# Optimization experiments

Hardware: AMD Instinct MI355X
Metric: run time of the kernel (lower is better)

The kernel has to match this reference:

```python
import jax, jax.numpy as jnp
import numpy as np

B, N = 1, 768
C_A, C_S, C_Z = 768, 384, 128
H, C_HID, N_TRANS = 16, 48, 2
INF = 1e9
PNAMES = ['attn_s_ln_g', 'attn_ada_gate_w', 'attn_ada_gate_b', 'attn_ada_skip_w',
          'wq', 'bq', 'wk', 'wv', 'z_ln_g', 'z_ln_b', 'wb', 'wg', 'wo',
          'attn_out_gate_w', 'attn_out_gate_b',
          'tr_s_ln_g', 'tr_ada_gate_w', 'tr_ada_gate_b', 'tr_ada_skip_w',
          'tr_w1', 'tr_w2', 'tr_wo', 'tr_out_gate_w', 'tr_out_gate_b']


def _ln(x, eps=1e-5):
    mu = jnp.mean(x, axis=-1, keepdims=True)
    var = jnp.mean((x - mu) ** 2, axis=-1, keepdims=True)
    return (x - mu) * jax.lax.rsqrt(var + eps)


def _adaln(a, s, s_g, gate_w, gate_b, skip_w):
    # AF3 Algorithm 26 AdaLN: a <- LN(a, no affine); s <- LN(s, scale only)
    a_ln = _ln(a)
    s_ln = _ln(s) * s_g
    return jax.nn.sigmoid(s_ln @ gate_w + gate_b) * a_ln + s_ln @ skip_w


def setup_inputs() -> dict:
    key = jax.random.key(0)
    ks = iter(jax.random.split(key, 40))
    w = lambda *sh: jax.random.normal(next(ks), sh, jnp.float32) * 0.02
    return dict(
        a=jax.random.normal(next(ks), (B, N, C_A), jnp.float32),
        s=jax.random.normal(next(ks), (B, N, C_S), jnp.float32),
        z=jax.random.normal(next(ks), (B, N, N, C_Z), jnp.float32),
        mask=jnp.ones((B, N), jnp.int32),
        attn_s_ln_g=jnp.ones((C_S,), jnp.float32),
        attn_ada_gate_w=w(C_S, C_A),
        attn_ada_gate_b=jnp.zeros((C_A,), jnp.float32),
        attn_ada_skip_w=w(C_S, C_A),
        wq=w(C_A, H * C_HID), bq=jnp.zeros((H * C_HID,), jnp.float32),
        wk=w(C_A, H * C_HID), wv=w(C_A, H * C_HID),
        z_ln_g=jnp.ones((C_Z,), jnp.float32), z_ln_b=jnp.zeros((C_Z,), jnp.float32),
        wb=w(C_Z, H), wg=w(C_A, H * C_HID), wo=w(H * C_HID, C_A),
        attn_out_gate_w=w(C_S, C_A),
        attn_out_gate_b=jnp.full((C_A,), -2.0, jnp.float32),  # AdaLN-Zero bias init -2
        tr_s_ln_g=jnp.ones((C_S,), jnp.float32),
        tr_ada_gate_w=w(C_S, C_A),
        tr_ada_gate_b=jnp.zeros((C_A,), jnp.float32),
        tr_ada_skip_w=w(C_S, C_A),
        tr_w1=w(C_A, N_TRANS * C_A), tr_w2=w(C_A, N_TRANS * C_A),
        tr_wo=w(N_TRANS * C_A, C_A),
        tr_out_gate_w=w(C_S, C_A),
        tr_out_gate_b=jnp.full((C_A,), -2.0, jnp.float32),
    )


def _block(a, s, z, maskf, p):
    # --- AttentionPairBias (AF3 Alg 24), residual ---
    a_ln = _adaln(a, s, p['attn_s_ln_g'], p['attn_ada_gate_w'],
                  p['attn_ada_gate_b'], p['attn_ada_skip_w'])
    q = (a_ln @ p['wq'] + p['bq']).reshape(B, N, H, C_HID)
    k = (a_ln @ p['wk']).reshape(B, N, H, C_HID)
    v = (a_ln @ p['wv']).reshape(B, N, H, C_HID)
    pair_bias = (_ln(z) * p['z_ln_g'] + p['z_ln_b']) @ p['wb']  # [B,N,N,H]
    logits = jnp.einsum('bqhc,bkhc->bhqk', q, k) / np.float32(np.sqrt(C_HID))
    logits = logits + jnp.moveaxis(pair_bias, -1, 1)
    logits = logits + (maskf - 1.0)[:, None, None, :] * INF  # mask over keys
    attn = jax.nn.softmax(logits, axis=-1)
    o = jnp.einsum('bhqk,bkhc->bqhc', attn, v)
    g = jax.nn.sigmoid(a_ln @ p['wg']).reshape(B, N, H, C_HID)
    o = (o * g).reshape(B, N, H * C_HID) @ p['wo']
    o = jax.nn.sigmoid(s @ p['attn_out_gate_w'] + p['attn_out_gate_b']) * o
    a = a + o
    # --- ConditionedTransitionBlock (AF3 Alg 25, SwiGLU), residual ---
    t_ln = _adaln(a, s, p['tr_s_ln_g'], p['tr_ada_gate_w'],
                  p['tr_ada_gate_b'], p['tr_ada_skip_w'])
    hid = jax.nn.silu(t_ln @ p['tr_w1']) * (t_ln @ p['tr_w2'])
    t = jax.nn.sigmoid(s @ p['tr_out_gate_w'] + p['tr_out_gate_b']) * (hid @ p['tr_wo'])
    t = t * maskf[..., None]  # _mask_trans=True
    return a + t


def reference(a, s, z, mask, attn_s_ln_g, attn_ada_gate_w, attn_ada_gate_b,
              attn_ada_skip_w, wq, bq, wk, wv, z_ln_g, z_ln_b, wb, wg, wo,
              attn_out_gate_w, attn_out_gate_b, tr_s_ln_g, tr_ada_gate_w,
              tr_ada_gate_b, tr_ada_skip_w, tr_w1, tr_w2, tr_wo,
              tr_out_gate_w, tr_out_gate_b):
    p = dict(zip(PNAMES, (attn_s_ln_g, attn_ada_gate_w, attn_ada_gate_b,
                          attn_ada_skip_w, wq, bq, wk, wv, z_ln_g, z_ln_b, wb,
                          wg, wo, attn_out_gate_w, attn_out_gate_b, tr_s_ln_g,
                          tr_ada_gate_w, tr_ada_gate_b, tr_ada_skip_w, tr_w1,
                          tr_w2, tr_wo, tr_out_gate_w, tr_out_gate_b)))
    return _block(a, s, z, mask.astype(a.dtype), p)
```

## Files before the change

### kernel.cpp

```cpp
#include <hip/hip_runtime.h>
#include <hip/hip_bf16.h>
#include <stdint.h>


typedef __bf16 bf16x8 __attribute__((ext_vector_type(8)));
typedef float  f32x4  __attribute__((ext_vector_type(4)));

#define DEVI __device__ __forceinline__

DEVI uint16_t f2b(float f){ __hip_bfloat16 h = __float2bfloat16(f); return __builtin_bit_cast(uint16_t, h); }
DEVI float    b2f(uint16_t u){ return __bfloat162float(__builtin_bit_cast(__hip_bfloat16, u)); }
DEVI float    sigm(float x){ return 1.0f/(1.0f + __expf(-x)); }

DEVI f32x4 MFMA(uint4 a, uint4 b, f32x4 c){
  return __builtin_amdgcn_mfma_f32_16x16x32_bf16(
      __builtin_bit_cast(bf16x8, a), __builtin_bit_cast(bf16x8, b), c, 0, 0, 0);
}

DEVI void glds16(const void* g, void* l){
  __builtin_amdgcn_global_load_lds(
      (const __attribute__((address_space(1))) void*)g,
      (__attribute__((address_space(3))) void*)l, 16, 0, 0);
}

constexpr size_t SZ_BT_ADA   = (size_t)1536*384*2;
constexpr size_t OFF_BT_ADA_ATTN = 0;
constexpr size_t OFF_BT_ADA_TR   = OFF_BT_ADA_ATTN + SZ_BT_ADA;
constexpr size_t OFF_BT_OUTGATE  = OFF_BT_ADA_TR   + SZ_BT_ADA;
constexpr size_t OFF_BT_QKVG     = OFF_BT_OUTGATE  + SZ_BT_ADA;
constexpr size_t OFF_BT_WO       = OFF_BT_QKVG + (size_t)3072*768*2;
constexpr size_t OFF_BT_W12      = OFF_BT_WO   + (size_t)768*768*2;
constexpr size_t OFF_BT_TRWO     = OFF_BT_W12  + (size_t)3072*768*2;
constexpr size_t OFF_WBGT        = OFF_BT_TRWO + (size_t)768*1536*2;
constexpr size_t OFF_ZCOL        = OFF_WBGT + 4096;
constexpr size_t OFF_OGB         = OFF_ZCOL + 256;
constexpr size_t OFF_SBF         = OFF_OGB + 6144;
constexpr size_t OFF_SLNA        = OFF_SBF  + (size_t)768*384*2;
constexpr size_t OFF_SLNT        = OFF_SLNA + (size_t)768*384*2;
constexpr size_t OFF_GATEOUT     = OFF_SLNT + (size_t)768*384*2;
constexpr size_t OFF_GSA         = OFF_GATEOUT + (size_t)768*1536*4;
constexpr size_t OFF_GST         = OFF_GSA + (size_t)768*1536*4;
constexpr size_t OFF_ALNBF       = OFF_GST + (size_t)768*1536*4;
constexpr size_t OFF_QP          = OFF_ALNBF + (size_t)768*768*2;
constexpr size_t OFF_KP          = OFF_QP + (size_t)16*768*48*2;
constexpr size_t OFF_VT          = OFF_KP + (size_t)16*768*48*2;
constexpr size_t OFF_GB          = OFF_VT + (size_t)16*48*768*2;
constexpr size_t OFF_BIASB       = OFF_GB + (size_t)768*768*2;
constexpr size_t OFF_OBF         = OFF_BIASB + (size_t)16*768*768*2;
constexpr size_t OFF_AMID        = OFF_OBF + (size_t)768*768*2;
constexpr size_t OFF_HID         = OFF_BIASB;

extern "C" size_t kernel_workspace_size(void){ return (size_t)64 << 20; }

DEVI void cvt_body(const float* src, uint16_t* dst, int K, int N, int il, int local,
                   float (*lds)[33])
{
  int t = threadIdx.x;
  int tN = N >> 5;
  int n0 = (local % tN) << 5, k0 = (local / tN) << 5;
  int c = t & 31, r0 = t >> 5;
  #pragma unroll
  for (int i = 0; i < 4; i++){
    int kk = r0 + 8*i;
    lds[kk][c] = src[(size_t)(k0+kk)*N + n0 + c];
  }
  __syncthreads();
  int rbase = (il == 0) ? n0 : (((n0 >> 5) << 6) + ((il == 2) ? 32 : 0));
  #pragma unroll
  for (int i = 0; i < 4; i++){
    int nn = r0 + 8*i;
    dst[(size_t)(rbase+nn)*K + k0 + c] = f2b(lds[c][nn]);
  }
}

struct PreArgs {
  const float* src[6];
  uint16_t*    dst[6];
  int K[6], N[6];
  int prefix[7];
  int n_cvt;
  const float *s, *g_attn, *g_tr, *aogb, *togb, *zg, *zb, *wb;
  uint16_t *s_bf, *sln_a, *sln_t;
  float* ogb; uint16_t* wbgt; float* zcol;
};

__global__ __launch_bounds__(256) void k_pre(PreArgs a){
  __shared__ float lds[32][33];
  __shared__ float rs_[4], rq_[4];
  int bid = blockIdx.x, t = threadIdx.x;
  if (bid < a.n_cvt){
    int ti = 0;
    while (ti < 5 && bid >= a.prefix[ti+1]) ti++;
    cvt_body(a.src[ti], a.dst[ti], a.K[ti], a.N[ti], 0, bid - a.prefix[ti], lds);
    return;
  }
  int b = bid - a.n_cvt;
  if (b < 384){
    int row_id = b*2 + (t >> 7);
    int tt = t & 127;
    const float* row = a.s + (size_t)row_id*384;
    float x0 = row[tt], x1 = row[tt+128], x2 = row[tt+256];
    float sm = x0+x1+x2, sq = x0*x0+x1*x1+x2*x2;
    #pragma unroll
    for (int off = 32; off; off >>= 1){ sm += __shfl_xor(sm, off, 64); sq += __shfl_xor(sq, off, 64); }
    int w = t >> 6;
    if ((t & 63) == 0){ rs_[w] = sm; rq_[w] = sq; }
    __syncthreads();
    int base = (t >> 7)*2;
    float S = rs_[base]+rs_[base+1], Q = rq_[base]+rq_[base+1];
    float mu = S * (1.f/384.f);
    float var = Q * (1.f/384.f) - mu*mu;
    float rstd = rsqrtf(var + 1e-5f);
    float xs[3] = {x0, x1, x2};
    #pragma unroll
    for (int i = 0; i < 3; i++){
      int ci = tt + 128*i;
      float ln = (xs[i] - mu) * rstd;
      a.s_bf [(size_t)row_id*384 + ci] = f2b(xs[i]);
      a.sln_a[(size_t)row_id*384 + ci] = f2b(ln * a.g_attn[ci]);
      a.sln_t[(size_t)row_id*384 + ci] = f2b(ln * a.g_tr[ci]);
    }
  } else if (b == 384){
    for (int i = t; i < 1536; i += 256)
      a.ogb[i] = (i < 768) ? a.aogb[i] : a.togb[i-768];
  } else {
    for (int i = t; i < 2048; i += 256){
      int h = i >> 7, c = i & 127;
      a.wbgt[i] = f2b(a.zg[c] * a.wb[c*16 + h]);
    }
    if (t < 16){
      float cs = 0.f, cn = 0.f;
      for (int c = 0; c < 128; c++){ cs += a.zg[c]*a.wb[c*16+t]; cn += a.zb[c]*a.wb[c*16+t]; }
      a.zcol[t] = cs; a.zcol[16+t] = cn;
    }
  }
}

struct GemmP {
  const uint16_t *A, *BT;
  int N, K, gx, mode, gateLd, gateOff;
  float* outF; uint16_t* outB;
  const float *bias, *gate, *resid;
  const int* mask;
  uint16_t *qp, *kp, *vt, *gb;
  const float* bq;
};

DEVI void gemm_body(const GemmP& p, int bx, int by, uint16_t* As, uint16_t* Bs){
  int t = threadIdx.x;
  int n0 = bx*64, m0 = by*64;
  int w = t >> 6, lane = t & 63, mm = lane & 15, q = lane >> 4;
  const uint16_t* gA[4]; const uint16_t* gB[4];
  uint16_t* lA[4]; uint16_t* lB[4];
  #pragma unroll
  for (int i = 0; i < 4; i++){
    int fc = 256*w + 64*i + lane;
    int r = fc >> 4, cc = (fc & 15) ^ (r & 7);
    gA[i] = p.A  + (size_t)(m0 + r)*p.K + cc*8;
    gB[i] = p.BT + (size_t)(n0 + r)*p.K + cc*8;
    lA[i] = As + (256*w + 64*i)*8;
    lB[i] = Bs + (256*w + 64*i)*8;
  }
  f32x4 zz = {0.f,0.f,0.f,0.f};
  f32x4 acc[4] = {zz, zz, zz, zz};
  int sw = mm & 7;
  for (int k0 = 0; k0 < p.K; k0 += 128){
    __syncthreads();
    #pragma unroll
    for (int i = 0; i < 4; i++){
      glds16(gA[i] + k0, lA[i]);
      glds16(gB[i] + k0, lB[i]);
    }
    __syncthreads();
    #pragma unroll
    for (int kc = 0; kc < 4; kc++){
      uint4 av = *(const uint4*)&As[(16*w + mm)*128 + ((kc*4 + q) ^ sw)*8];
      #pragma unroll
      for (int j = 0; j < 4; j++){
        uint4 bv = *(const uint4*)&Bs[(16*j + mm)*128 + ((kc*4 + q) ^ sw)*8];
        acc[j] = MFMA(av, bv, acc[j]);
      }
    }
  }
  if (p.mode == 6){
    #pragma unroll
    for (int jj = 0; jj < 2; jj++){
      #pragma unroll
      for (int rr = 0; rr < 4; rr++){
        int row = m0 + 16*w + q*4 + rr;
        int col = (n0 >> 1) + 16*jj + mm;
        float x1 = acc[jj][rr], x2 = acc[jj+2][rr];
        p.outB[(size_t)row*(p.N >> 1) + col] = f2b(x1*sigm(x1)*x2);
      }
    }
    return;
  }
  if (p.mode == 7 && n0 >= 1536 && n0 < 2304){
    __syncthreads();
    #pragma unroll
    for (int j = 0; j < 4; j++)
      #pragma unroll
      for (int rr = 0; rr < 4; rr++)
        As[(16*j + mm)*72 + (16*w + q*4 + rr)] = f2b(acc[j][rr]);
    __syncthreads();
    int cl = t >> 2, ch = (t & 3)*16;
    int gc = n0 - 1536 + cl, h = gc/48, c = gc - 48*h;
    uint16_t* dst = p.vt + ((size_t)h*48 + c)*768 + m0 + ch;
    *(uint4*)dst       = *(const uint4*)&As[cl*72 + ch];
    *(uint4*)(dst + 8) = *(const uint4*)&As[cl*72 + ch + 8];
    return;
  }
  const float scale = 0.14433756729740643f;
  #pragma unroll
  for (int j = 0; j < 4; j++){
    #pragma unroll
    for (int rr = 0; rr < 4; rr++){
      int row = m0 + 16*w + q*4 + rr;
      int col = n0 + 16*j + mm;
      float v = acc[j][rr];
      size_t oi = (size_t)row*p.N + col;
      if (p.mode == 0)      p.outF[oi] = v;
      else if (p.mode == 2) p.outF[oi] = sigm(v + p.bias[col]);
      else if (p.mode == 5) p.outF[oi] = p.resid[oi] + p.gate[(size_t)row*p.gateLd + p.gateOff + col]*v;
      else if (p.mode == 4){
        float mf = (float)p.mask[row];
        p.outF[oi] = p.resid[oi] + mf * p.gate[(size_t)row*p.gateLd + p.gateOff + col] * v;
      } else {
        if (col < 768){
          int h = col/48, c = col - h*48;
          p.qp[((size_t)h*768 + row)*48 + c] = f2b((v + p.bq[col])*scale);
        } else if (col < 1536){
          int cc = col - 768; int h = cc/48, c = cc - h*48;
          p.kp[((size_t)h*768 + row)*48 + c] = f2b(v);
        } else {
          p.gb[(size_t)row*768 + (col - 2304)] = f2b(v);
        }
      }
    }
  }
}

__global__ __launch_bounds__(256) void k_gemm(GemmP p){
  __shared__ __align__(16) uint16_t AsBs[2*64*128];
  gemm_body(p, blockIdx.x, blockIdx.y, AsBs, AsBs + 64*128);
}

DEVI void zbias_body(const float* __restrict__ z, const uint16_t* __restrict__ wbgt_g,
                     const float* __restrict__ zcol, uint16_t* __restrict__ bias_g,
                     int zbid, uint16_t* zb, uint16_t* wbt, float* mu_s, float* rs_s,
                     uint16_t* Sout)
{
  int t = threadIdx.x;
  int bx = zbid % 12, by = zbid / 12;
  size_t P0 = (size_t)by*768 + (size_t)bx*64;
  ((uint4*)wbt)[t] = ((const uint4*)wbgt_g)[t];
  int p = t >> 2, qq = t & 3;
  const float4* zp = (const float4*)(z + (P0 + p)*128) + qq*8;
  float s1 = 0.f, s2 = 0.f;
  uint32_t lb[16];
  #pragma unroll
  for (int it = 0; it < 8; it++){
    float4 v = zp[it];
    s1 += v.x + v.y + v.z + v.w;
    s2 += v.x*v.x + v.y*v.y + v.z*v.z + v.w*v.w;
    lb[2*it]   = (uint32_t)f2b(v.x) | ((uint32_t)f2b(v.y) << 16);
    lb[2*it+1] = (uint32_t)f2b(v.z) | ((uint32_t)f2b(v.w) << 16);
  }
  uint4* zb4 = (uint4*)zb;
  #pragma unroll
  for (int kk = 0; kk < 4; kk++)
    zb4[p*16 + qq*4 + kk] = ((uint4*)lb)[kk];
  s1 += __shfl_xor(s1, 1, 64); s1 += __shfl_xor(s1, 2, 64);
  s2 += __shfl_xor(s2, 1, 64); s2 += __shfl_xor(s2, 2, 64);
  if (qq == 0){
    float mu = s1 * (1.f/128.f);
    mu_s[p] = mu;
    rs_s[p] = rsqrtf(s2*(1.f/128.f) - mu*mu + 1e-5f);
  }
  __syncthreads();
  int w = t >> 6, lane = t & 63, hh = lane & 15, q = lane >> 4;
  float cs = zcol[hh], cn = zcol[16 + hh];
  f32x4 acc = {0.f, 0.f, 0.f, 0.f};
  const uint4* wbt4 = (const uint4*)wbt;
  #pragma unroll
  for (int kc = 0; kc < 4; kc++){
    uint4 av = zb4[(16*w + hh)*16 + kc*4 + q];
    uint4 bv = wbt4[hh*16 + kc*4 + q];
    acc = MFMA(av, bv, acc);
  }
  #pragma unroll
  for (int rr = 0; rr < 4; rr++){
    int pl = 16*w + q*4 + rr;
    float val = rs_s[pl]*(acc[rr] - mu_s[pl]*cs) + cn;
    Sout[hh*72 + pl] = f2b(val);
  }
  __syncthreads();
  int h2 = t >> 4, p2 = (t & 15)*4;
  uint2 v2 = *(uint2*)&Sout[h2*72 + p2];
  *(uint2*)(bias_g + (size_t)h2*589824 + P0 + p2) = v2;
}

struct ZbP { const float* z; const uint16_t* wbgt; const float* zcol; uint16_t* biasb; int off; };
struct CvtP {
  const float* src[8];
  uint16_t* dst[8];
  int K[8], N[8], il[8];
  int prefix[9];
  int n;
};
struct FatArgs {
  GemmP g[3];
  int gstart[4];
  int gn, gtotal, ztotal;
  ZbP zb;
  CvtP cv;
};

union __align__(16) MegaLds {
  struct { uint16_t As[64*128], Bs[64*128]; } g;
  struct { uint16_t zb[64*128]; uint16_t wbt[16*128]; float mu[64], rs[64]; uint16_t Sout[16*72]; } z;
  float cv[32][33];
};

__global__ __launch_bounds__(256) void k_mega(FatArgs fa){
  __shared__ MegaLds L;
  int bid = blockIdx.x;
  if (bid < fa.gtotal){
    int gi = 0;
    while (gi + 1 < fa.gn && bid >= fa.gstart[gi+1]) gi++;
    GemmP p = fa.g[gi];
    int local = bid - fa.gstart[gi];
    gemm_body(p, local % p.gx, local / p.gx, L.g.As, L.g.Bs);
    return;
  }
  if (bid < fa.gtotal + fa.ztotal){
    zbias_body(fa.zb.z, fa.zb.wbgt, fa.zb.zcol, fa.zb.biasb, fa.zb.off + (bid - fa.gtotal),
               L.z.zb, L.z.wbt, L.z.mu, L.z.rs, L.z.Sout);
    return;
  }
  int cid = bid - fa.gtotal - fa.ztotal;
  int ti = 0;
  while (ti + 1 < fa.cv.n && cid >= fa.cv.prefix[ti+1]) ti++;
  cvt_body(fa.cv.src[ti], fa.cv.dst[ti], fa.cv.K[ti], fa.cv.N[ti], fa.cv.il[ti],
           cid - fa.cv.prefix[ti], L.cv);
}

__global__ __launch_bounds__(256) void k_adaln2(
    const float* __restrict__ asrc, const float* __restrict__ gs,
    const float* __restrict__ gb, uint16_t* __restrict__ out)
{
  int b = blockIdx.x, t = threadIdx.x;
  const float* row = asrc + (size_t)b*768;
  float x0 = row[t], x1 = row[t+256], x2 = row[t+512];
  float sm = x0+x1+x2, sq = x0*x0+x1*x1+x2*x2;
  #pragma unroll
  for (int off = 32; off; off >>= 1){ sm += __shfl_xor(sm, off, 64); sq += __shfl_xor(sq, off, 64); }
  __shared__ float rs_[4], rq_[4];
  int w = t >> 6;
  if ((t & 63) == 0){ rs_[w] = sm; rq_[w] = sq; }
  __syncthreads();
  float S = rs_[0]+rs_[1]+rs_[2]+rs_[3], Q = rq_[0]+rq_[1]+rq_[2]+rq_[3];
  float mu = S*(1.f/768.f), var = Q*(1.f/768.f) - mu*mu, rstd = rsqrtf(var + 1e-5f);
  float xs[3] = {x0, x1, x2};
  #pragma unroll
  for (int i = 0; i < 3; i++){
    int c = t + 256*i;
    float g  = gs[(size_t)b*1536 + c];
    float sk = gs[(size_t)b*1536 + 768 + c];
    out[(size_t)b*768 + c] = f2b(sigm(g + gb[c]) * ((xs[i]-mu)*rstd) + sk);
  }
}

__global__ __launch_bounds__(256) void k_flash(
    const uint16_t* __restrict__ qp, const uint16_t* __restrict__ kp,
    const uint16_t* __restrict__ vt, const uint16_t* __restrict__ bias_g,
    const uint16_t* __restrict__ gb, const int* __restrict__ mask,
    uint16_t* __restrict__ obf)
{
  __shared__ __align__(16) uint16_t Qs[64*72], Ks[64*72], Vs[48*72], Ps[64*72], Bi[64*72];
  __shared__ float mk[768];
  int t = threadIdx.x;
  int q0 = blockIdx.x*64, h = blockIdx.y;
  int w = t >> 6, lane = t & 63, mm = lane & 15, q = lane >> 4;
  {
    const uint16_t* qbase = qp + ((size_t)h*768 + q0)*48;
    for (int i = t; i < 384; i += 256){
      int r = i/6, ch = i - r*6;
      *(uint4*)&Qs[r*72 + ch*8] = *(const uint4*)&qbase[r*48 + ch*8];
    }
    if (t < 128){
      uint4 z4; z4.x = z4.y = z4.z = z4.w = 0u;
      int r = t >> 1, off = 48 + (t & 1)*8;
      *(uint4*)&Qs[r*72 + off] = z4;
      *(uint4*)&Ks[r*72 + off] = z4;
    }
    mk[t] = (float)mask[t]; mk[t+256] = (float)mask[t+256]; mk[t+512] = (float)mask[t+512];
  }
  f32x4 zz = {0.f,0.f,0.f,0.f};
  f32x4 o0 = zz, o1 = zz, o2 = zz;
  f32x4 m_i = {-1e30f,-1e30f,-1e30f,-1e30f};
  f32x4 l_i = zz;
  const uint16_t* bbase0 = bias_g + (size_t)h*589824 + (size_t)q0*768;
  for (int kt = 0; kt < 12; kt++){
    __syncthreads();
    {
      const uint16_t* kbase = kp + ((size_t)h*768 + kt*64)*48;
      for (int i = t; i < 384; i += 256){
        int r = i/6, ch = i - r*6;
        *(uint4*)&Ks[r*72 + ch*8] = *(const uint4*)&kbase[r*48 + ch*8];
      }
      const uint16_t* vbase = vt + (size_t)h*48*768 + kt*64;
      for (int i = t; i < 384; i += 256){
        int r = i >> 3, ch = i & 7;
        *(uint4*)&Vs[r*72 + ch*8] = *(const uint4*)&vbase[(size_t)r*768 + ch*8];
      }
      const uint16_t* bbase = bbase0 + kt*64;
      for (int i = t; i < 512; i += 256){
        int r = i >> 3, ch = i & 7;
        *(uint4*)&Bi[r*72 + ch*8] = *(const uint4*)&bbase[(size_t)r*768 + ch*8];
      }
    }
    __syncthreads();
    f32x4 s[4] = {zz, zz, zz, zz};
    #pragma unroll
    for (int kc = 0; kc < 2; kc++){
      uint4 av = *(const uint4*)&Qs[(16*w + mm)*72 + kc*32 + q*8];
      #pragma unroll
      for (int j = 0; j < 4; j++){
        uint4 bv = *(const uint4*)&Ks[(16*j + mm)*72 + kc*32 + q*8];
        s[j] = MFMA(av, bv, s[j]);
      }
    }
    int rbase = 16*w + q*4;
    #pragma unroll
    for (int j = 0; j < 4; j++){
      int scol = kt*64 + 16*j + mm;
      float mt = (mk[scol] - 1.f)*1e9f;
      #pragma unroll
      for (int rr = 0; rr < 4; rr++)
        s[j][rr] += b2f(Bi[(rbase+rr)*72 + 16*j + mm]) + mt;
    }
    f32x4 tm = s[0];
    #pragma unroll
    for (int j = 1; j < 4; j++)
      #pragma unroll
      for (int rr = 0; rr < 4; rr++) tm[rr] = fmaxf(tm[rr], s[j][rr]);
    #pragma unroll
    for (int off = 1; off < 16; off <<= 1)
      #pragma unroll
      for (int rr = 0; rr < 4; rr++) tm[rr] = fmaxf(tm[rr], __shfl_xor(tm[rr], off, 64));
    f32x4 mnew, alpha, rsum = zz;
    #pragma unroll
    for (int rr = 0; rr < 4; rr++){
      mnew[rr] = fmaxf(m_i[rr], tm[rr]);
      alpha[rr] = __expf(m_i[rr] - mnew[rr]);
    }
    #pragma unroll
    for (int j = 0; j < 4; j++)
      #pragma unroll
      for (int rr = 0; rr < 4; rr++){
        s[j][rr] = __expf(s[j][rr] - mnew[rr]);
        rsum[rr] += s[j][rr];
      }
    #pragma unroll
    for (int off = 1; off < 16; off <<= 1)
      #pragma unroll
      for (int rr = 0; rr < 4; rr++) rsum[rr] += __shfl_xor(rsum[rr], off, 64);
    #pragma unroll
    for (int rr = 0; rr < 4; rr++){
      l_i[rr] = l_i[rr]*alpha[rr] + rsum[rr];
      o0[rr] *= alpha[rr]; o1[rr] *= alpha[rr]; o2[rr] *= alpha[rr];
      m_i[rr] = mnew[rr];
    }
    #pragma unroll
    for (int j = 0; j < 4; j++)
      #pragma unroll
      for (int rr = 0; rr < 4; rr++)
        Ps[(16*w + q*4 + rr)*72 + 16*j + mm] = f2b(s[j][rr]);
    __syncthreads();
    #pragma unroll
    for (int kc = 0; kc < 2; kc++){
      uint4 av = *(const uint4*)&Ps[(16*w + mm)*72 + kc*32 + q*8];
      uint4 bv0 = *(const uint4*)&Vs[(mm)*72      + kc*32 + q*8];
      uint4 bv1 = *(const uint4*)&Vs[(16+mm)*72   + kc*32 + q*8];
      uint4 bv2 = *(const uint4*)&Vs[(32+mm)*72   + kc*32 + q*8];
      o0 = MFMA(av, bv0, o0);
      o1 = MFMA(av, bv1, o1);
      o2 = MFMA(av, bv2, o2);
    }
  }
  f32x4 inv;
  #pragma unroll
  for (int rr = 0; rr < 4; rr++) inv[rr] = 1.f / l_i[rr];
  #pragma unroll
  for (int j = 0; j < 3; j++){
    f32x4 ov = (j == 0) ? o0 : (j == 1) ? o1 : o2;
    int col = 16*j + mm;
    #pragma unroll
    for (int rr = 0; rr < 4; rr++){
      int row = q0 + 16*w + q*4 + rr;
      float g = b2f(gb[(size_t)row*768 + h*48 + col]);
      obf[(size_t)row*768 + h*48 + col] = f2b(ov[rr]*inv[rr]*sigm(g));
    }
  }
}

extern "C" void kernel_launch(void* const* d_in, const int* in_sizes, int n_in,
                              void* d_out, int out_size, void* d_ws, size_t ws_size,
                              hipStream_t stream)
{
  const float* a            = (const float*)d_in[0];
  const float* s            = (const float*)d_in[1];
  const float* z            = (const float*)d_in[2];
  const int*   mask         = (const int*)  d_in[3];
  const float* attn_s_ln_g  = (const float*)d_in[4];
  const float* attn_gate_w  = (const float*)d_in[5];
  const float* attn_gate_b  = (const float*)d_in[6];
  const float* attn_skip_w  = (const float*)d_in[7];
  const float* wq           = (const float*)d_in[8];
  const float* bq           = (const float*)d_in[9];
  const float* wk           = (const float*)d_in[10];
  const float* wv           = (const float*)d_in[11];
  const float* z_ln_g       = (const float*)d_in[12];
  const float* z_ln_b       = (const float*)d_in[13];
  const float* wb           = (const float*)d_in[14];
  const float* wg           = (const float*)d_in[15];
  const float* wo           = (const float*)d_in[16];
  const float* attn_og_w    = (const float*)d_in[17];
  const float* attn_og_b    = (const float*)d_in[18];
  const float* tr_s_ln_g    = (const float*)d_in[19];
  const float* tr_gate_w    = (const float*)d_in[20];
  const float* tr_gate_b    = (const float*)d_in[21];
  const float* tr_skip_w    = (const float*)d_in[22];
  const float* tr_w1        = (const float*)d_in[23];
  const float* tr_w2        = (const float*)d_in[24];
  const float* tr_wo        = (const float*)d_in[25];
  const float* tr_og_w      = (const float*)d_in[26];
  const float* tr_og_b      = (const float*)d_in[27];

  char* wsb = (char*)d_ws;
  uint16_t* BTa   = (uint16_t*)(wsb + OFF_BT_ADA_ATTN);
  uint16_t* BTt   = (uint16_t*)(wsb + OFF_BT_ADA_TR);
  uint16_t* BTo   = (uint16_t*)(wsb + OFF_BT_OUTGATE);
  uint16_t* BTq   = (uint16_t*)(wsb + OFF_BT_QKVG);
  uint16_t* BTwo  = (uint16_t*)(wsb + OFF_BT_WO);
  uint16_t* BTw12 = (uint16_t*)(wsb + OFF_BT_W12);
  uint16_t* BTtw  = (uint16_t*)(wsb + OFF_BT_TRWO);
  uint16_t* WBGT  = (uint16_t*)(wsb + OFF_WBGT);
  float*    ZCOL  = (float*)   (wsb + OFF_ZCOL);
  float*    OGB   = (float*)   (wsb + OFF_OGB);
  uint16_t* SBF   = (uint16_t*)(wsb + OFF_SBF);
  uint16_t* SLNA  = (uint16_t*)(wsb + OFF_SLNA);
  uint16_t* SLNT  = (uint16_t*)(wsb + OFF_SLNT);
  float*    GATEOUT=(float*)   (wsb + OFF_GATEOUT);
  float*    GSA   = (float*)   (wsb + OFF_GSA);
  float*    GST   = (float*)   (wsb + OFF_GST);
  uint16_t* ALNBF = (uint16_t*)(wsb + OFF_ALNBF);
  uint16_t* QP    = (uint16_t*)(wsb + OFF_QP);
  uint16_t* KP    = (uint16_t*)(wsb + OFF_KP);
  uint16_t* VT    = (uint16_t*)(wsb + OFF_VT);
  uint16_t* GB    = (uint16_t*)(wsb + OFF_GB);
  uint16_t* BIASB = (uint16_t*)(wsb + OFF_BIASB);
  uint16_t* OBF   = (uint16_t*)(wsb + OFF_OBF);
  float*    AMID  = (float*)   (wsb + OFF_AMID);
  uint16_t* HIDBF = (uint16_t*)(wsb + OFF_HID);
  float*    OUTF  = (float*)d_out;

  PreArgs pa;
  {
    const float* srcs[6] = {attn_gate_w, attn_skip_w, tr_gate_w, tr_skip_w, attn_og_w, tr_og_w};
    uint16_t* dsts[6] = {BTa, BTa + (size_t)768*384, BTt, BTt + (size_t)768*384,
                         BTo, BTo + (size_t)768*384};
    int pre = 0;
    for (int i = 0; i < 6; i++){
      pa.src[i] = srcs[i]; pa.dst[i] = dsts[i]; pa.K[i] = 384; pa.N[i] = 768;
      pa.prefix[i] = pre; pre += 288;
    }
    pa.prefix[6] = pre;
    pa.n_cvt = pre;
  }
  pa.s = s; pa.g_attn = attn_s_ln_g; pa.g_tr = tr_s_ln_g;
  pa.aogb = attn_og_b; pa.togb = tr_og_b;
  pa.zg = z_ln_g; pa.zb = z_ln_b; pa.wb = wb;
  pa.s_bf = SBF; pa.sln_a = SLNA; pa.sln_t = SLNT;
  pa.ogb = OGB; pa.wbgt = WBGT; pa.zcol = ZCOL;
  k_pre<<<pa.n_cvt + 386, 256, 0, stream>>>(pa);

  FatArgs f2{};
  {
    GemmP p{};
    p.A = SBF; p.BT = BTo; p.N = 1536; p.K = 384; p.gx = 24; p.mode = 2;
    p.outF = GATEOUT; p.bias = OGB;
    f2.g[0] = p;
    p = GemmP{};
    p.A = SLNA; p.BT = BTa; p.N = 1536; p.K = 384; p.gx = 24; p.mode = 0; p.outF = GSA;
    f2.g[1] = p;
    p = GemmP{};
    p.A = SLNT; p.BT = BTt; p.N = 1536; p.K = 384; p.gx = 24; p.mode = 0; p.outF = GST;
    f2.g[2] = p;
    f2.gstart[0] = 0; f2.gstart[1] = 288; f2.gstart[2] = 576; f2.gstart[3] = 864;
    f2.gn = 3; f2.gtotal = 864;
    f2.ztotal = 4608;
    f2.zb = ZbP{z, WBGT, ZCOL, BIASB, 0};
    const float* csrc[8] = {wq, wk, wv, wg, wo, tr_w1, tr_w2, tr_wo};
    uint16_t* cdst[8] = {BTq, BTq + (size_t)768*768, BTq + (size_t)2*768*768, BTq + (size_t)3*768*768,
                         BTwo, BTw12, BTw12, BTtw};
    int cK[8] = {768,768,768,768,768, 768,768, 1536};
    int cN[8] = {768,768,768,768,768, 1536,1536, 768};
    int cil[8] = {0,0,0,0,0, 1,2, 0};
    int ct[8]  = {576,576,576,576,576, 1152,1152, 1152};
    int cpre = 0;
    for (int i = 0; i < 8; i++){
      f2.cv.src[i] = csrc[i]; f2.cv.dst[i] = cdst[i];
      f2.cv.K[i] = cK[i]; f2.cv.N[i] = cN[i]; f2.cv.il[i] = cil[i];
      f2.cv.prefix[i] = cpre; cpre += ct[i];
    }
    f2.cv.prefix[8] = cpre;
    f2.cv.n = 8;
    k_mega<<<864 + 4608 + cpre, 256, 0, stream>>>(f2);
  }

  k_adaln2<<<768, 256, 0, stream>>>(a, GSA, attn_gate_b, ALNBF);

  FatArgs f4{};
  {
    GemmP p{};
    p.A = ALNBF; p.BT = BTq; p.N = 3072; p.K = 768; p.gx = 48; p.mode = 7;
    p.qp = QP; p.kp = KP; p.vt = VT; p.gb = GB; p.bq = bq;
    f4.g[0] = p;
    f4.gstart[0] = 0; f4.gstart[1] = 576; f4.gn = 1; f4.gtotal = 576;
    f4.ztotal = 4608;
    f4.zb = ZbP{z, WBGT, ZCOL, BIASB, 4608};
    f4.cv.n = 0;
    k_mega<<<576 + 4608, 256, 0, stream>>>(f4);
  }

  k_flash<<<dim3(12,16), 256, 0, stream>>>(QP, KP, VT, BIASB, GB, mask, OBF);

  {
    GemmP p{};
    p.A = OBF; p.BT = BTwo; p.N = 768; p.K = 768; p.gx = 12; p.mode = 5;
    p.outF = AMID; p.gate = GATEOUT; p.gateLd = 1536; p.gateOff = 0; p.resid = a;
    k_gemm<<<dim3(12,12), 256, 0, stream>>>(p);
  }

  k_adaln2<<<768, 256, 0, stream>>>(AMID, GST, tr_gate_b, ALNBF);

  {
    GemmP p{};
    p.A = ALNBF; p.BT = BTw12; p.N = 3072; p.K = 768; p.gx = 48; p.mode = 6;
    p.outB = HIDBF;
    k_gemm<<<dim3(48,12), 256, 0, stream>>>(p);
  }

  {
    GemmP p{};
    p.A = HIDBF; p.BT = BTtw; p.N = 768; p.K = 1536; p.gx = 12; p.mode = 4;
    p.outF = OUTF; p.gate = GATEOUT; p.gateLd = 1536; p.gateOff = 768;
    p.resid = AMID; p.mask = mask;
    k_gemm<<<dim3(12,12), 256, 0, stream>>>(p);
  }
}
```

Baseline: 588.2 us.

## Fuse attention AdaLN into gate GEMM epilogue, store gates as bf16, prefetch flash tiles

Computes the LayerNorm of `a` in the pre-kernel and interleaves the attention AdaLN gate and skip weights, so the gate GEMM epilogue directly produces the bf16 AdaLN output. This removes one k_adaln2 launch and its fp32 round trip. Gate outputs and transition gate/skip projections are now stored in bf16 instead of fp32, halving that memory traffic at some precision cost. The flash kernel now register-prefetches the next K/V/bias tile during compute of the current one.

New measurement: 578.7 us. Within noise of the previous version (-1.6%).

```diff
diff --git a/kernel.cpp b/kernel.cpp
--- a/kernel.cpp
+++ b/kernel.cpp
@@ -38,8 +38,8 @@
 constexpr size_t OFF_SLNA        = OFF_SBF  + (size_t)768*384*2;
 constexpr size_t OFF_SLNT        = OFF_SLNA + (size_t)768*384*2;
 constexpr size_t OFF_GATEOUT     = OFF_SLNT + (size_t)768*384*2;
-constexpr size_t OFF_GSA         = OFF_GATEOUT + (size_t)768*1536*4;
-constexpr size_t OFF_GST         = OFF_GSA + (size_t)768*1536*4;
+constexpr size_t OFF_LNA         = OFF_GATEOUT + (size_t)768*1536*4;
+constexpr size_t OFF_GST         = OFF_LNA + (size_t)768*1536*4;
 constexpr size_t OFF_ALNBF       = OFF_GST + (size_t)768*1536*4;
 constexpr size_t OFF_QP          = OFF_ALNBF + (size_t)768*768*2;
 constexpr size_t OFF_KP          = OFF_QP + (size_t)16*768*48*2;
@@ -76,11 +76,11 @@
 struct PreArgs {
   const float* src[6];
   uint16_t*    dst[6];
-  int K[6], N[6];
+  int K[6], N[6], il[6];
   int prefix[7];
   int n_cvt;
-  const float *s, *g_attn, *g_tr, *aogb, *togb, *zg, *zb, *wb;
-  uint16_t *s_bf, *sln_a, *sln_t;
+  const float *s, *g_attn, *g_tr, *aogb, *togb, *zg, *zb, *wb, *ain;
+  uint16_t *s_bf, *sln_a, *sln_t, *lna;
   float* ogb; uint16_t* wbgt; float* zcol;
 };
 
@@ -91,7 +91,7 @@
   if (bid < a.n_cvt){
     int ti = 0;
     while (ti < 5 && bid >= a.prefix[ti+1]) ti++;
-    cvt_body(a.src[ti], a.dst[ti], a.K[ti], a.N[ti], 0, bid - a.prefix[ti], lds);
+    cvt_body(a.src[ti], a.dst[ti], a.K[ti], a.N[ti], a.il[ti], bid - a.prefix[ti], lds);
     return;
   }
   int b = bid - a.n_cvt;
@@ -123,7 +123,7 @@
   } else if (b == 384){
     for (int i = t; i < 1536; i += 256)
       a.ogb[i] = (i < 768) ? a.aogb[i] : a.togb[i-768];
-  } else {
+  } else if (b == 385){
     for (int i = t; i < 2048; i += 256){
       int h = i >> 7, c = i & 127;
       a.wbgt[i] = f2b(a.zg[c] * a.wb[c*16 + h]);
@@ -133,6 +133,22 @@
       for (int c = 0; c < 128; c++){ cs += a.zg[c]*a.wb[c*16+t]; cn += a.zb[c]*a.wb[c*16+t]; }
       a.zcol[t] = cs; a.zcol[16+t] = cn;
     }
+  } else {
+    int row = b - 386;
+    const float* rp = a.ain + (size_t)row*768;
+    float x0 = rp[t], x1 = rp[t+256], x2 = rp[t+512];
+    float sm = x0+x1+x2, sq = x0*x0+x1*x1+x2*x2;
+    #pragma unroll
+    for (int off = 32; off; off >>= 1){ sm += __shfl_xor(sm, off, 64); sq += __shfl_xor(sq, off, 64); }
+    int w = t >> 6;
+    if ((t & 63) == 0){ rs_[w] = sm; rq_[w] = sq; }
+    __syncthreads();
+    float S = rs_[0]+rs_[1]+rs_[2]+rs_[3], Q = rq_[0]+rq_[1]+rq_[2]+rq_[3];
+    float mu = S*(1.f/768.f), var = Q*(1.f/768.f) - mu*mu, rstd = rsqrtf(var + 1e-5f);
+    float xs[3] = {x0, x1, x2};
+    #pragma unroll
+    for (int i = 0; i < 3; i++)
+      a.lna[(size_t)row*768 + t + 256*i] = f2b((xs[i]-mu)*rstd);
   }
 }
 
@@ -140,7 +156,8 @@
   const uint16_t *A, *BT;
   int N, K, gx, mode, gateLd, gateOff;
   float* outF; uint16_t* outB;
-  const float *bias, *gate, *resid;
+  const float *bias, *resid;
+  const uint16_t *gate, *lna;
   const int* mask;
   uint16_t *qp, *kp, *vt, *gb;
   const float* bq;
@@ -195,6 +212,20 @@
     }
     return;
   }
+  if (p.mode == 8){
+    #pragma unroll
+    for (int jj = 0; jj < 2; jj++){
+      #pragma unroll
+      for (int rr = 0; rr < 4; rr++){
+        int row = m0 + 16*w + q*4 + rr;
+        int col = (n0 >> 1) + 16*jj + mm;
+        float xg = acc[jj][rr], xs2 = acc[jj+2][rr];
+        float ln = b2f(p.lna[(size_t)row*768 + col]);
+        p.outB[(size_t)row*768 + col] = f2b(sigm(xg + p.bias[col])*ln + xs2);
+      }
+    }
+    return;
+  }
   if (p.mode == 7 && n0 >= 1536 && n0 < 2304){
     __syncthreads();
     #pragma unroll
@@ -220,11 +251,13 @@
       float v = acc[j][rr];
       size_t oi = (size_t)row*p.N + col;
       if (p.mode == 0)      p.outF[oi] = v;
-      else if (p.mode == 2) p.outF[oi] = sigm(v + p.bias[col]);
-      else if (p.mode == 5) p.outF[oi] = p.resid[oi] + p.gate[(size_t)row*p.gateLd + p.gateOff + col]*v;
+      else if (p.mode == 1) p.outB[oi] = f2b(v);
+      else if (p.mode == 3) p.outB[oi] = f2b(sigm(v + p.bias[col]));
+      else if (p.mode == 5)
+        p.outF[oi] = p.resid[oi] + b2f(p.gate[(size_t)row*p.gateLd + p.gateOff + col])*v;
       else if (p.mode == 4){
         float mf = (float)p.mask[row];
-        p.outF[oi] = p.resid[oi] + mf * p.gate[(size_t)row*p.gateLd + p.gateOff + col] * v;
+        p.outF[oi] = p.resid[oi] + mf * b2f(p.gate[(size_t)row*p.gateLd + p.gateOff + col]) * v;
       } else {
         if (col < 768){
           int h = col/48, c = col - h*48;
@@ -346,7 +379,7 @@
 }
 
 __global__ __launch_bounds__(256) void k_adaln2(
-    const float* __restrict__ asrc, const float* __restrict__ gs,
+    const float* __restrict__ asrc, const uint16_t* __restrict__ gs,
     const float* __restrict__ gb, uint16_t* __restrict__ out)
 {
   int b = blockIdx.x, t = threadIdx.x;
@@ -365,8 +398,8 @@
   #pragma unroll
   for (int i = 0; i < 3; i++){
     int c = t + 256*i;
-    float g  = gs[(size_t)b*1536 + c];
-    float sk = gs[(size_t)b*1536 + 768 + c];
+    float g  = b2f(gs[(size_t)b*1536 + c]);
+    float sk = b2f(gs[(size_t)b*1536 + 768 + c]);
     out[(size_t)b*768 + c] = f2b(sigm(g + gb[c]) * ((xs[i]-mu)*rstd) + sk);
   }
 }
@@ -396,31 +429,46 @@
     }
     mk[t] = (float)mask[t]; mk[t+256] = (float)mask[t+256]; mk[t+512] = (float)mask[t+512];
   }
+  const uint16_t* sbase[5]; int sstep[5]; uint16_t* sdst[5];
+  const uint16_t* bbase0 = bias_g + (size_t)h*589824 + (size_t)q0*768;
+  #pragma unroll
+  for (int i2 = 0; i2 < 5; i2++){
+    int c = t + 256*i2;
+    if (c < 384){
+      int r = c/6, ch = c - 6*r;
+      sbase[i2] = kp + ((size_t)h*768 + r)*48 + ch*8;
+      sstep[i2] = 64*48;
+      sdst[i2]  = &Ks[r*72 + ch*8];
+    } else if (c < 768){
+      int i3 = c - 384; int r = i3 >> 3, ch = i3 & 7;
+      sbase[i2] = vt + ((size_t)h*48 + r)*768 + ch*8;
+      sstep[i2] = 64;
+      sdst[i2]  = &Vs[r*72 + ch*8];
+    } else {
+      int i3 = c - 768; int r = i3 >> 3, ch = i3 & 7;
+      sbase[i2] = bbase0 + (size_t)r*768 + ch*8;
+      sstep[i2] = 64;
+      sdst[i2]  = &Bi[r*72 + ch*8];
+    }
+  }
+  uint4 pre[5];
+  #pragma unroll
+  for (int i2 = 0; i2 < 5; i2++) pre[i2] = *(const uint4*)sbase[i2];
+
   f32x4 zz = {0.f,0.f,0.f,0.f};
   f32x4 o0 = zz, o1 = zz, o2 = zz;
   f32x4 m_i = {-1e30f,-1e30f,-1e30f,-1e30f};
   f32x4 l_i = zz;
-  const uint16_t* bbase0 = bias_g + (size_t)h*589824 + (size_t)q0*768;
   for (int kt = 0; kt < 12; kt++){
     __syncthreads();
-    {
-      const uint16_t* kbase = kp + ((size_t)h*768 + kt*64)*48;
-      for (int i = t; i < 384; i += 256){
-        int r = i/6, ch = i - r*6;
-        *(uint4*)&Ks[r*72 + ch*8] = *(const uint4*)&kbase[r*48 + ch*8];
-      }
-      const uint16_t* vbase = vt + (size_t)h*48*768 + kt*64;
-      for (int i = t; i < 384; i += 256){
-        int r = i >> 3, ch = i & 7;
-        *(uint4*)&Vs[r*72 + ch*8] = *(const uint4*)&vbase[(size_t)r*768 + ch*8];
-      }
-      const uint16_t* bbase = bbase0 + kt*64;
-      for (int i = t; i < 512; i += 256){
-        int r = i >> 3, ch = i & 7;
-        *(uint4*)&Bi[r*72 + ch*8] = *(const uint4*)&bbase[(size_t)r*768 + ch*8];
-      }
-    }
-    __syncthreads();
+    #pragma unroll
+    for (int i2 = 0; i2 < 5; i2++) *(uint4*)sdst[i2] = pre[i2];
+    __syncthreads();
+    if (kt < 11){
+      #pragma unroll
+      for (int i2 = 0; i2 < 5; i2++)
+        pre[i2] = *(const uint4*)(sbase[i2] + (size_t)(kt+1)*sstep[i2]);
+    }
     f32x4 s[4] = {zz, zz, zz, zz};
     #pragma unroll
     for (int kc = 0; kc < 2; kc++){
@@ -552,9 +600,9 @@
   uint16_t* SBF   = (uint16_t*)(wsb + OFF_SBF);
   uint16_t* SLNA  = (uint16_t*)(wsb + OFF_SLNA);
   uint16_t* SLNT  = (uint16_t*)(wsb + OFF_SLNT);
-  float*    GATEOUT=(float*)   (wsb + OFF_GATEOUT);
-  float*    GSA   = (float*)   (wsb + OFF_GSA);
-  float*    GST   = (float*)   (wsb + OFF_GST);
+  uint16_t* GATEOUTB = (uint16_t*)(wsb + OFF_GATEOUT);
+  uint16_t* LNABF = (uint16_t*)(wsb + OFF_LNA);
+  uint16_t* GSTB  = (uint16_t*)(wsb + OFF_GST);
   uint16_t* ALNBF = (uint16_t*)(wsb + OFF_ALNBF);
   uint16_t* QP    = (uint16_t*)(wsb + OFF_QP);
   uint16_t* KP    = (uint16_t*)(wsb + OFF_KP);
@@ -569,11 +617,12 @@
   PreArgs pa;
   {
     const float* srcs[6] = {attn_gate_w, attn_skip_w, tr_gate_w, tr_skip_w, attn_og_w, tr_og_w};
-    uint16_t* dsts[6] = {BTa, BTa + (size_t)768*384, BTt, BTt + (size_t)768*384,
+    uint16_t* dsts[6] = {BTa, BTa, BTt, BTt + (size_t)768*384,
                          BTo, BTo + (size_t)768*384};
+    int ils[6] = {1, 2, 0, 0, 0, 0};
     int pre = 0;
     for (int i = 0; i < 6; i++){
-      pa.src[i] = srcs[i]; pa.dst[i] = dsts[i]; pa.K[i] = 384; pa.N[i] = 768;
+      pa.src[i] = srcs[i]; pa.dst[i] = dsts[i]; pa.K[i] = 384; pa.N[i] = 768; pa.il[i] = ils[i];
       pa.prefix[i] = pre; pre += 288;
     }
     pa.prefix[6] = pre;
@@ -581,22 +630,23 @@
   }
   pa.s = s; pa.g_attn = attn_s_ln_g; pa.g_tr = tr_s_ln_g;
   pa.aogb = attn_og_b; pa.togb = tr_og_b;
-  pa.zg = z_ln_g; pa.zb = z_ln_b; pa.wb = wb;
-  pa.s_bf = SBF; pa.sln_a = SLNA; pa.sln_t = SLNT;
+  pa.zg = z_ln_g; pa.zb = z_ln_b; pa.wb = wb; pa.ain = a;
+  pa.s_bf = SBF; pa.sln_a = SLNA; pa.sln_t = SLNT; pa.lna = LNABF;
   pa.ogb = OGB; pa.wbgt = WBGT; pa.zcol = ZCOL;
-  k_pre<<<pa.n_cvt + 386, 256, 0, stream>>>(pa);
+  k_pre<<<pa.n_cvt + 386 + 768, 256, 0, stream>>>(pa);
 
   FatArgs f2{};
   {
     GemmP p{};
-    p.A = SBF; p.BT = BTo; p.N = 1536; p.K = 384; p.gx = 24; p.mode = 2;
-    p.outF = GATEOUT; p.bias = OGB;
+    p.A = SBF; p.BT = BTo; p.N = 1536; p.K = 384; p.gx = 24; p.mode = 3;
+    p.outB = GATEOUTB; p.bias = OGB;
     f2.g[0] = p;
     p = GemmP{};
-    p.A = SLNA; p.BT = BTa; p.N = 1536; p.K = 384; p.gx = 24; p.mode = 0; p.outF = GSA;
+    p.A = SLNA; p.BT = BTa; p.N = 1536; p.K = 384; p.gx = 24; p.mode = 8;
+    p.outB = ALNBF; p.bias = attn_gate_b; p.lna = LNABF;
     f2.g[1] = p;
     p = GemmP{};
-    p.A = SLNT; p.BT = BTt; p.N = 1536; p.K = 384; p.gx = 24; p.mode = 0; p.outF = GST;
+    p.A = SLNT; p.BT = BTt; p.N = 1536; p.K = 384; p.gx = 24; p.mode = 1; p.outB = GSTB;
     f2.g[2] = p;
     f2.gstart[0] = 0; f2.gstart[1] = 288; f2.gstart[2] = 576; f2.gstart[3] = 864;
     f2.gn = 3; f2.gtotal = 864;
@@ -620,8 +670,6 @@
     k_mega<<<864 + 4608 + cpre, 256, 0, stream>>>(f2);
   }
 
-  k_adaln2<<<768, 256, 0, stream>>>(a, GSA, attn_gate_b, ALNBF);
-
   FatArgs f4{};
   {
     GemmP p{};
@@ -640,11 +688,11 @@
   {
     GemmP p{};
     p.A = OBF; p.BT = BTwo; p.N = 768; p.K = 768; p.gx = 12; p.mode = 5;
-    p.outF = AMID; p.gate = GATEOUT; p.gateLd = 1536; p.gateOff = 0; p.resid = a;
+    p.outF = AMID; p.gate = GATEOUTB; p.gateLd = 1536; p.gateOff = 0; p.resid = a;
     k_gemm<<<dim3(12,12), 256, 0, stream>>>(p);
   }
 
-  k_adaln2<<<768, 256, 0, stream>>>(AMID, GST, tr_gate_b, ALNBF);
+  k_adaln2<<<768, 256, 0, stream>>>(AMID, GSTB, tr_gate_b, ALNBF);
 
   {
     GemmP p{};
@@ -656,7 +704,7 @@
   {
     GemmP p{};
     p.A = HIDBF; p.BT = BTtw; p.N = 768; p.K = 1536; p.gx = 12; p.mode = 4;
-    p.outF = OUTF; p.gate = GATEOUT; p.gateLd = 1536; p.gateOff = 768;
+    p.outF = OUTF; p.gate = GATEOUTB; p.gateLd = 1536; p.gateOff = 768;
     p.resid = AMID; p.mask = mask;
     k_gemm<<<dim3(12,12), 256, 0, stream>>>(p);
   }
```
